# Optimization experiments

Hardware: AMD Instinct MI355X
Metric: run time of the kernel (lower is better)

Reference implementation:

```python
import jax, jax.numpy as jnp
import numpy as np


def setup_inputs() -> dict:
    key = jax.random.key(0)
    ks = jax.random.split(key, 8)
    B, C, H, W = 8, 256, 64, 64
    r = 32  # channels // reduction
    return {
        "x": jax.random.normal(ks[0], (B, C, H, W), dtype=jnp.float32),
        "wq": jax.random.normal(ks[1], (r, C), dtype=jnp.float32) * 0.02,
        "bq": jax.random.normal(ks[2], (r,), dtype=jnp.float32) * 0.02,
        "wk": jax.random.normal(ks[3], (r, C), dtype=jnp.float32) * 0.02,
        "bk": jax.random.normal(ks[4], (r,), dtype=jnp.float32) * 0.02,
        "wv": jax.random.normal(ks[5], (C, C), dtype=jnp.float32) * 0.02,
        "bv": jax.random.normal(ks[6], (C,), dtype=jnp.float32) * 0.02,
        "gamma": jax.random.normal(ks[7], (1,), dtype=jnp.float32),
    }


def reference(x, wq, bq, wk, bk, wv, bv, gamma):
    B, C, H, W = x.shape
    N = H * W
    r = wq.shape[0]
    scale = r ** (-0.5)
    xf = x.reshape(B, C, N)  # flatten spatial tokens
    # 1x1 convs == per-pixel linear projections
    q = jnp.einsum("rc,bcn->bnr", wq, xf) + bq  # (B, N, r)
    k = jnp.einsum("rc,bcn->brn", wk, xf) + bk[:, None]  # (B, r, N)
    v = jnp.einsum("dc,bcn->bdn", wv, xf) + bv[:, None]  # (B, C, N)
    attn = jax.nn.softmax(jnp.einsum("bnr,brm->bnm", q, k) * scale, axis=-1)  # (B, N, N)
    # out[b,c,n] = sum_m v[b,c,m] * attn[b,n,m]
    out = jnp.einsum("bdm,bnm->bdn", v, attn).reshape(B, C, H, W)
    return x + gamma[0] * out
```

## Files before the change

kernel.cpp:

```cpp
#include <hip/hip_runtime.h>
#include <hip/hip_bf16.h>


typedef float  f32x4   __attribute__((ext_vector_type(4)));
typedef short  short8  __attribute__((ext_vector_type(8)));
typedef unsigned short ushort4v __attribute__((ext_vector_type(4)));
typedef unsigned short ushort8v __attribute__((ext_vector_type(8)));

__device__ __forceinline__ unsigned short f2bf(float f) {
    __hip_bfloat16 h = __float2bfloat16(f);
    return __builtin_bit_cast(unsigned short, h);
}

__global__ __launch_bounds__(256) void wconv_kernel(
    const float* __restrict__ wq, const float* __restrict__ wk,
    const float* __restrict__ wv, unsigned short* __restrict__ Wall)
{
    int i4 = blockIdx.x * 256 + threadIdx.x;
    int e = i4 * 4;
    const float* src; int off;
    if (e < 8192)       { src = wq; off = e; }
    else if (e < 16384) { src = wk; off = e - 8192; }
    else                { src = wv; off = e - 16384; }
    f32x4 v = *(const f32x4*)(src + off);
    ushort4v u;
#pragma unroll
    for (int j = 0; j < 4; ++j) u[j] = f2bf(v[j]);
    *(ushort4v*)(Wall + e) = u;
}

__global__ __launch_bounds__(256) void xpose_kernel(
    const float* __restrict__ x, unsigned short* __restrict__ xT, int C, int N)
{
    const int t  = threadIdx.x;
    const int n  = blockIdx.x * 256 + t;
    const int c0 = blockIdx.y * 64;
    const int b  = blockIdx.z;
    const float* xb = x + ((size_t)b * C + c0) * N + n;

    unsigned short tmp[64];
#pragma unroll
    for (int i = 0; i < 64; ++i)
        tmp[i] = f2bf(xb[(size_t)i * N]);

    unsigned short* dst = xT + ((size_t)b * N + n) * 256 + c0;
#pragma unroll
    for (int i = 0; i < 8; ++i) {
        ushort8v u;
#pragma unroll
        for (int j = 0; j < 8; ++j) u[j] = tmp[i * 8 + j];
        *(ushort8v*)(dst + i * 8) = u;
    }
}

__global__ __launch_bounds__(256) void projmm_kernel(
    const unsigned short* __restrict__ xT,
    const unsigned short* __restrict__ Wall,
    const float* __restrict__ bq, const float* __restrict__ bk,
    const float* __restrict__ bv,
    unsigned short* __restrict__ qa,
    unsigned short* __restrict__ ka,
    unsigned char* __restrict__ vt8,
    int N, float scale)
{
    __shared__ __align__(16) unsigned short xs[64 * 136];
    __shared__ __align__(16) unsigned short ws[64 * 136];

    const int t  = threadIdx.x;
    const int l  = t & 63;
    const int w  = t >> 6;
    const int qi = l & 15;
    const int g  = l >> 4;
    const int n0 = blockIdx.x * 64;
    const int o0 = blockIdx.y * 64;
    const int b  = blockIdx.z;
    const int tile = n0 >> 6;
    const unsigned short* xTb = xT + (size_t)b * N * 256;

    const f32x4 zero4 = {0.f, 0.f, 0.f, 0.f};
    f32x4 acc[4];
#pragma unroll
    for (int nf = 0; nf < 4; ++nf) acc[nf] = zero4;

    for (int kp = 0; kp < 2; ++kp) {
        if (kp) __syncthreads();
        for (int it = w; it < 34; it += 4) {
            int isw = it >= 17;
            int it2 = isw ? it - 17 : it;
            unsigned short* lbase = (isw ? ws : xs) + it2 * 512;
            int ch  = it2 * 64 + l;
            int row = ch / 17;
            int c16 = ch - row * 17;
            int cc  = c16 > 15 ? 15 : c16;
            const unsigned short* src = isw
                ? (Wall + (size_t)(o0 + row) * 256 + kp * 128 + cc * 8)
                : (xTb + (size_t)(n0 + row) * 256 + kp * 128 + cc * 8);
            __builtin_amdgcn_global_load_lds(
                (const __attribute__((address_space(1))) unsigned int*)src,
                (__attribute__((address_space(3))) unsigned int*)lbase, 16, 0, 0);
        }
        __syncthreads();

#pragma unroll
        for (int ks = 0; ks < 4; ++ks) {
            short8 af;
            {
                const unsigned short* ap = ws + (w * 16 + qi) * 136 + ks * 32 + g * 4;
                ushort4v lo = *(const ushort4v*)ap;
                ushort4v hi = *(const ushort4v*)(ap + 16);
#pragma unroll
                for (int j = 0; j < 4; ++j) { af[j] = (short)lo[j]; af[4 + j] = (short)hi[j]; }
            }
#pragma unroll
            for (int nf = 0; nf < 4; ++nf) {
                short8 bf;
                const unsigned short* bp = xs + (nf * 16 + qi) * 136 + ks * 32 + g * 4;
                ushort4v lo = *(const ushort4v*)bp;
                ushort4v hi = *(const ushort4v*)(bp + 16);
#pragma unroll
                for (int j = 0; j < 4; ++j) { bf[j] = (short)lo[j]; bf[4 + j] = (short)hi[j]; }
                acc[nf] = __builtin_amdgcn_mfma_f32_16x16x32_bf16(af, bf, acc[nf], 0, 0, 0);
            }
        }
    }

    if (o0 == 0) {
        const float* bias = (w < 2) ? bq : bk;
        float sc = (w < 2) ? scale : 1.0f;
        unsigned short* dst = (w < 2) ? qa : ka;
#pragma unroll
        for (int nf = 0; nf < 4; ++nf) {
            ushort4v u;
#pragma unroll
            for (int j = 0; j < 4; ++j) {
                int r = (w & 1) * 16 + g * 4 + j;
                u[j] = f2bf((acc[nf][j] + bias[r]) * sc);
            }
            *(ushort4v*)(dst + ((((size_t)b * 64 + tile) * 4 + nf) * 64 + g * 16 + qi) * 8 + (w & 1) * 4) = u;
        }
    } else {
        unsigned char* vtb = vt8 + ((size_t)b * 64 + tile) * 16384;
#pragma unroll
        for (int nf = 0; nf < 4; ++nf) {
            int m = nf * 16 + qi;
            int G   = ((m & 32) ? 4 : 0) + ((m >> 2) & 3);
            int pos = ((m >> 4) & 1) * 4 + (m & 3);
#pragma unroll
            for (int j = 0; j < 4; ++j) {
                int c = o0 - 64 + w * 16 + g * 4 + j;
                int r = __builtin_amdgcn_cvt_pk_fp8_f32(acc[nf][j] + bv[c], 0.f, 0, false);
                vtb[(size_t)c * 64 + ((G ^ ((c >> 1) & 7)) << 3) + pos] = (unsigned char)(r & 0xFF);
            }
        }
    }
}

__global__ __launch_bounds__(512, 4) void attn_kernel(
    const float* __restrict__ x,
    const unsigned short* __restrict__ qa,
    const unsigned short* __restrict__ ka,
    const unsigned char* __restrict__ vt8,
    const float* __restrict__ gamma,
    float* __restrict__ out, int C, int N)
{
    __shared__ __align__(16) unsigned char vs[4][20480];

    const int t  = threadIdx.x;
    const int l  = t & 63;
    const int w  = t >> 6;
    const int qi = l & 15;
    const int g  = l >> 4;
    const int qg = w & 3;
    const int kh = w >> 2;
    const int tile_q = blockIdx.x;
    const int b  = blockIdx.y;

    const f32x4 zero4 = {0.f, 0.f, 0.f, 0.f};

    short8 qfrag = *(const short8*)(
        qa + ((((size_t)b * 64 + tile_q) * 4 + qg) * 64 + l) * 8);

    const unsigned char* kab_b = (const unsigned char*)(ka + ((size_t)b * 64) * 2048);
    const unsigned char* vtb   = vt8 + ((size_t)b * 64) * 16384;

    auto stage = [&](int buf, int tl) {
        const unsigned char* vsrc = vtb + (size_t)tl * 16384 + w * 2048 + l * 16;
        unsigned char* vdst = &vs[buf][w * 2048 + l * 16];
        __builtin_amdgcn_global_load_lds(
            (const __attribute__((address_space(1))) unsigned int*)vsrc,
            (__attribute__((address_space(3))) unsigned int*)vdst, 16, 0, 0);
        __builtin_amdgcn_global_load_lds(
            (const __attribute__((address_space(1))) unsigned int*)(vsrc + 1024),
            (__attribute__((address_space(3))) unsigned int*)(vdst + 1024), 16, 0, 0);
        const unsigned char* ksrc = kab_b + (size_t)tl * 4096 + w * 512 + l * 4;
        unsigned char* kdst = &vs[buf][16384 + w * 512 + l * 4];
        __builtin_amdgcn_global_load_lds(
            (const __attribute__((address_space(1))) unsigned int*)ksrc,
            (__attribute__((address_space(3))) unsigned int*)kdst, 4, 0, 0);
        __builtin_amdgcn_global_load_lds(
            (const __attribute__((address_space(1))) unsigned int*)(ksrc + 256),
            (__attribute__((address_space(3))) unsigned int*)(kdst + 256), 4, 0, 0);
    };

    f32x4 o_[16];
#pragma unroll
    for (int cf = 0; cf < 16; ++cf) o_[cf] = zero4;
    float lsum = 0.f;
    long acur = 0;

    auto packP = [&](const f32x4& s0, const f32x4& s1) -> long {
        float p[8];
#pragma unroll
        for (int j = 0; j < 4; ++j) { p[j] = __expf(s0[j]); p[4 + j] = __expf(s1[j]); }
#pragma unroll
        for (int j = 0; j < 8; ++j) lsum += p[j];
        int w0 = __builtin_amdgcn_cvt_pk_fp8_f32(p[0], p[1], 0, false);
        w0 = __builtin_amdgcn_cvt_pk_fp8_f32(p[2], p[3], w0, true);
        int w1 = __builtin_amdgcn_cvt_pk_fp8_f32(p[4], p[5], 0, false);
        w1 = __builtin_amdgcn_cvt_pk_fp8_f32(p[6], p[7], w1, true);
        return (long)(((unsigned long long)(unsigned int)w0) |
                      ((unsigned long long)(unsigned int)w1 << 32));
    };

    const int voff = (((kh << 2) | g) ^ ((qi >> 1) & 7)) << 3;
    auto pv = [&](int buf) {
        const unsigned char* vrow = &vs[buf][qi * 64 + voff];
#pragma unroll
        for (int cf = 0; cf < 16; ++cf) {
            long v8 = *(const long*)(vrow + cf * 1024);
            o_[cf] = __builtin_amdgcn_mfma_f32_16x16x32_fp8_fp8(acur, v8, o_[cf], 0, 0, 0);
        }
    };

    stage(0, 0);
    stage(1, 1);

    for (int tl = 0; tl < 64; ++tl) {
        asm volatile("s_waitcnt vmcnt(4)\n\ts_barrier" ::: "memory");
        __builtin_amdgcn_sched_barrier(0);

        if (tl < 62) stage((tl + 2) & 3, tl + 2);

        const unsigned char* kb2 = &vs[tl & 3][16384 + kh * 2048 + l * 16];
        short8 kf0 = *(const short8*)kb2;
        short8 kf1 = *(const short8*)(kb2 + 1024);
        f32x4 s0 = __builtin_amdgcn_mfma_f32_16x16x32_bf16(kf0, qfrag, zero4, 0, 0, 0);
        f32x4 s1 = __builtin_amdgcn_mfma_f32_16x16x32_bf16(kf1, qfrag, zero4, 0, 0, 0);

        if (tl) pv((tl - 1) & 3);

        acur = packP(s0, s1);
    }
    pv(3);

    float l_run = lsum;
    l_run += __shfl_xor(l_run, 16);
    l_run += __shfl_xor(l_run, 32);

    __syncthreads();
    float* cbuf = (float*)vs;
    float* lex  = cbuf + 8192;
    const int lx = l & 31;
    float* bp = cbuf + ((qg * 64) + l) * 32;
    if (kh == 1) {
        lex[qg * 64 + l] = l_run;
#pragma unroll
        for (int cf = 0; cf < 8; ++cf)
#pragma unroll
            for (int j = 0; j < 4; ++j) bp[(cf * 4 + j) ^ lx] = o_[cf][j];
    }
    __syncthreads();

    float cj[4];
    const float gm = gamma[0];
    const float* xb = x + (size_t)b * C * N;
    float* ob = out + (size_t)b * C * N;
    const int ncol = tile_q * 64 + qg * 16 + g * 4;

    if (kh == 0) {
        float lt = l_run + lex[qg * 64 + l];
        float c0 = gm / lt;
#pragma unroll
        for (int j = 0; j < 4; ++j) cj[j] = __shfl(c0, g * 4 + j);
#pragma unroll
        for (int cf = 0; cf < 8; ++cf) {
            int c = cf * 16 + qi;
            f32x4 xv = *(const f32x4*)(xb + (size_t)c * N + ncol);
            f32x4 ov;
#pragma unroll
            for (int j = 0; j < 4; ++j)
                ov[j] = xv[j] + (o_[cf][j] + bp[(cf * 4 + j) ^ lx]) * cj[j];
            *(f32x4*)(ob + (size_t)c * N + ncol) = ov;
        }
    }
    __syncthreads();

    if (kh == 1) {
#pragma unroll
        for (int cf = 0; cf < 8; ++cf)
#pragma unroll
            for (int j = 0; j < 4; ++j) bp[(cf * 4 + j) ^ lx] = o_[8 + cf][j];
    }
    __syncthreads();

    if (kh == 0) {
#pragma unroll
        for (int cf = 0; cf < 8; ++cf) {
            int c = (8 + cf) * 16 + qi;
            f32x4 xv = *(const f32x4*)(xb + (size_t)c * N + ncol);
            f32x4 ov;
#pragma unroll
            for (int j = 0; j < 4; ++j)
                ov[j] = xv[j] + (o_[8 + cf][j] + bp[(cf * 4 + j) ^ lx]) * cj[j];
            *(f32x4*)(ob + (size_t)c * N + ncol) = ov;
        }
    }
}

extern "C" void kernel_launch(void* const* d_in, const int* in_sizes, int n_in,
                              void* d_out, int out_size, void* d_ws, size_t ws_size,
                              hipStream_t stream) {
    const float* x     = (const float*)d_in[0];
    const float* wq    = (const float*)d_in[1];
    const float* bq    = (const float*)d_in[2];
    const float* wk    = (const float*)d_in[3];
    const float* bk    = (const float*)d_in[4];
    const float* wv    = (const float*)d_in[5];
    const float* bv    = (const float*)d_in[6];
    const float* gamma = (const float*)d_in[7];
    float* out = (float*)d_out;

    const int B = 8, C = 256, N = 4096;
    const float scale = 0.17677669529663687f;

    unsigned short* qa   = (unsigned short*)d_ws;
    unsigned short* ka   = qa + (size_t)B * 64 * 4 * 64 * 8;
    unsigned short* xT   = ka + (size_t)B * 64 * 4 * 64 * 8;
    unsigned short* Wall = xT + (size_t)B * N * 256;
    unsigned char*  vt8  = (unsigned char*)(Wall + 81920);

    wconv_kernel<<<80, 256, 0, stream>>>(wq, wk, wv, Wall);
    xpose_kernel<<<dim3(N / 256, C / 64, B), 256, 0, stream>>>(x, xT, C, N);
    projmm_kernel<<<dim3(N / 64, 5, B), 256, 0, stream>>>(
        xT, Wall, bq, bk, bv, qa, ka, vt8, N, scale);
    attn_kernel<<<dim3(N / 64, B), 512, 0, stream>>>(x, qa, ka, vt8, gamma, out, C, N);
}
```

Before: 109.7 us.

## Fuse x transpose/bf16 convert into projection kernel with double-buffered weights

Removes the separate transpose kernel and its bf16 xT intermediate buffer. The projection kernel now reads fp32 x directly, converts it to bf16 into a full-K shared tile, and loops over all five output blocks inside one workgroup. Weight tiles are double-buffered so the next slice loads while the current one is multiplied. The grid shrinks by 5x, which reduces parallelism, and the strided fp32 loads of x may coalesce less well.

```diff
diff --git a/kernel.cpp b/kernel.cpp
--- a/kernel.cpp
+++ b/kernel.cpp
@@ -29,32 +29,8 @@
     *(ushort4v*)(Wall + e) = u;
 }
 
-__global__ __launch_bounds__(256) void xpose_kernel(
-    const float* __restrict__ x, unsigned short* __restrict__ xT, int C, int N)
-{
-    const int t  = threadIdx.x;
-    const int n  = blockIdx.x * 256 + t;
-    const int c0 = blockIdx.y * 64;
-    const int b  = blockIdx.z;
-    const float* xb = x + ((size_t)b * C + c0) * N + n;
-
-    unsigned short tmp[64];
-#pragma unroll
-    for (int i = 0; i < 64; ++i)
-        tmp[i] = f2bf(xb[(size_t)i * N]);
-
-    unsigned short* dst = xT + ((size_t)b * N + n) * 256 + c0;
-#pragma unroll
-    for (int i = 0; i < 8; ++i) {
-        ushort8v u;
-#pragma unroll
-        for (int j = 0; j < 8; ++j) u[j] = tmp[i * 8 + j];
-        *(ushort8v*)(dst + i * 8) = u;
-    }
-}
-
 __global__ __launch_bounds__(256) void projmm_kernel(
-    const unsigned short* __restrict__ xT,
+    const float* __restrict__ x,
     const unsigned short* __restrict__ Wall,
     const float* __restrict__ bq, const float* __restrict__ bk,
     const float* __restrict__ bv,
@@ -63,8 +39,8 @@
     unsigned char* __restrict__ vt8,
     int N, float scale)
 {
-    __shared__ __align__(16) unsigned short xs[64 * 136];
-    __shared__ __align__(16) unsigned short ws[64 * 136];
+    __shared__ __align__(16) unsigned short xs[64 * 272];
+    __shared__ __align__(16) unsigned short ws2[2][64 * 136];
 
     const int t  = threadIdx.x;
     const int l  = t & 63;
@@ -72,40 +48,57 @@
     const int qi = l & 15;
     const int g  = l >> 4;
     const int n0 = blockIdx.x * 64;
-    const int o0 = blockIdx.y * 64;
-    const int b  = blockIdx.z;
+    const int b  = blockIdx.y;
     const int tile = n0 >> 6;
-    const unsigned short* xTb = xT + (size_t)b * N * 256;
-
-    const f32x4 zero4 = {0.f, 0.f, 0.f, 0.f};
-    f32x4 acc[4];
-#pragma unroll
-    for (int nf = 0; nf < 4; ++nf) acc[nf] = zero4;
-
-    for (int kp = 0; kp < 2; ++kp) {
-        if (kp) __syncthreads();
-        for (int it = w; it < 34; it += 4) {
-            int isw = it >= 17;
-            int it2 = isw ? it - 17 : it;
-            unsigned short* lbase = (isw ? ws : xs) + it2 * 512;
-            int ch  = it2 * 64 + l;
+
+    {
+        const float* xb = x + ((size_t)b * 256 + w * 64) * N + n0 + l;
+        unsigned short* dst = xs + l * 272 + w * 64;
+#pragma unroll
+        for (int i = 0; i < 8; ++i) {
+            ushort8v u;
+#pragma unroll
+            for (int j = 0; j < 8; ++j)
+                u[j] = f2bf(xb[(size_t)(i * 8 + j) * N]);
+            *(ushort8v*)(dst + i * 8) = u;
+        }
+    }
+
+    auto stageW = [&](int pb, int p) {
+        int ob = p >> 1, kp = p & 1;
+        for (int it = w; it < 17; it += 4) {
+            unsigned short* lbase = ws2[pb] + it * 512;
+            int ch  = it * 64 + l;
             int row = ch / 17;
             int c16 = ch - row * 17;
             int cc  = c16 > 15 ? 15 : c16;
-            const unsigned short* src = isw
-                ? (Wall + (size_t)(o0 + row) * 256 + kp * 128 + cc * 8)
-                : (xTb + (size_t)(n0 + row) * 256 + kp * 128 + cc * 8);
+            const unsigned short* src = Wall + (size_t)(ob * 64 + row) * 256 + kp * 128 + cc * 8;
             __builtin_amdgcn_global_load_lds(
                 (const __attribute__((address_space(1))) unsigned int*)src,
                 (__attribute__((address_space(3))) unsigned int*)lbase, 16, 0, 0);
         }
-        __syncthreads();
-
+    };
+
+    const f32x4 zero4 = {0.f, 0.f, 0.f, 0.f};
+    f32x4 acc[4];
+
+    stageW(0, 0);
+    __syncthreads();
+
+    for (int p = 0; p < 10; ++p) {
+        const int ob = p >> 1, kp = p & 1;
+        if (p < 9) stageW((p + 1) & 1, p + 1);
+        if (kp == 0) {
+#pragma unroll
+            for (int nf = 0; nf < 4; ++nf) acc[nf] = zero4;
+        }
+
+        const unsigned short* wsb = ws2[p & 1];
 #pragma unroll
         for (int ks = 0; ks < 4; ++ks) {
             short8 af;
             {
-                const unsigned short* ap = ws + (w * 16 + qi) * 136 + ks * 32 + g * 4;
+                const unsigned short* ap = wsb + (w * 16 + qi) * 136 + ks * 32 + g * 4;
                 ushort4v lo = *(const ushort4v*)ap;
                 ushort4v hi = *(const ushort4v*)(ap + 16);
 #pragma unroll
@@ -114,7 +107,7 @@
 #pragma unroll
             for (int nf = 0; nf < 4; ++nf) {
                 short8 bf;
-                const unsigned short* bp = xs + (nf * 16 + qi) * 136 + ks * 32 + g * 4;
+                const unsigned short* bp = xs + (nf * 16 + qi) * 272 + kp * 128 + ks * 32 + g * 4;
                 ushort4v lo = *(const ushort4v*)bp;
                 ushort4v hi = *(const ushort4v*)(bp + 16);
 #pragma unroll
@@ -122,36 +115,39 @@
                 acc[nf] = __builtin_amdgcn_mfma_f32_16x16x32_bf16(af, bf, acc[nf], 0, 0, 0);
             }
         }
-    }
-
-    if (o0 == 0) {
-        const float* bias = (w < 2) ? bq : bk;
-        float sc = (w < 2) ? scale : 1.0f;
-        unsigned short* dst = (w < 2) ? qa : ka;
-#pragma unroll
-        for (int nf = 0; nf < 4; ++nf) {
-            ushort4v u;
-#pragma unroll
-            for (int j = 0; j < 4; ++j) {
-                int r = (w & 1) * 16 + g * 4 + j;
-                u[j] = f2bf((acc[nf][j] + bias[r]) * sc);
+
+        if (kp == 1) {
+            if (ob == 0) {
+                const float* bias = (w < 2) ? bq : bk;
+                float sc = (w < 2) ? scale : 1.0f;
+                unsigned short* dst = (w < 2) ? qa : ka;
+#pragma unroll
+                for (int nf = 0; nf < 4; ++nf) {
+                    ushort4v u;
+#pragma unroll
+                    for (int j = 0; j < 4; ++j) {
+                        int r = (w & 1) * 16 + g * 4 + j;
+                        u[j] = f2bf((acc[nf][j] + bias[r]) * sc);
+                    }
+                    *(ushort4v*)(dst + ((((size_t)b * 64 + tile) * 4 + nf) * 64 + g * 16 + qi) * 8 + (w & 1) * 4) = u;
+                }
+            } else {
+                unsigned char* vtb = vt8 + ((size_t)b * 64 + tile) * 16384;
+#pragma unroll
+                for (int nf = 0; nf < 4; ++nf) {
+                    int m = nf * 16 + qi;
+                    int G   = ((m & 32) ? 4 : 0) + ((m >> 2) & 3);
+                    int pos = ((m >> 4) & 1) * 4 + (m & 3);
+#pragma unroll
+                    for (int j = 0; j < 4; ++j) {
+                        int c = (ob - 1) * 64 + w * 16 + g * 4 + j;
+                        int r = __builtin_amdgcn_cvt_pk_fp8_f32(acc[nf][j] + bv[c], 0.f, 0, false);
+                        vtb[(size_t)c * 64 + ((G ^ ((c >> 1) & 7)) << 3) + pos] = (unsigned char)(r & 0xFF);
+                    }
+                }
             }
-            *(ushort4v*)(dst + ((((size_t)b * 64 + tile) * 4 + nf) * 64 + g * 16 + qi) * 8 + (w & 1) * 4) = u;
-        }
-    } else {
-        unsigned char* vtb = vt8 + ((size_t)b * 64 + tile) * 16384;
-#pragma unroll
-        for (int nf = 0; nf < 4; ++nf) {
-            int m = nf * 16 + qi;
-            int G   = ((m & 32) ? 4 : 0) + ((m >> 2) & 3);
-            int pos = ((m >> 4) & 1) * 4 + (m & 3);
-#pragma unroll
-            for (int j = 0; j < 4; ++j) {
-                int c = o0 - 64 + w * 16 + g * 4 + j;
-                int r = __builtin_amdgcn_cvt_pk_fp8_f32(acc[nf][j] + bv[c], 0.f, 0, false);
-                vtb[(size_t)c * 64 + ((G ^ ((c >> 1) & 7)) << 3) + pos] = (unsigned char)(r & 0xFF);
-            }
-        }
+        }
+        __syncthreads();
     }
 }
 
@@ -335,13 +331,11 @@
 
     unsigned short* qa   = (unsigned short*)d_ws;
     unsigned short* ka   = qa + (size_t)B * 64 * 4 * 64 * 8;
-    unsigned short* xT   = ka + (size_t)B * 64 * 4 * 64 * 8;
-    unsigned short* Wall = xT + (size_t)B * N * 256;
+    unsigned short* Wall = ka + (size_t)B * 64 * 4 * 64 * 8;
     unsigned char*  vt8  = (unsigned char*)(Wall + 81920);
 
     wconv_kernel<<<80, 256, 0, stream>>>(wq, wk, wv, Wall);
-    xpose_kernel<<<dim3(N / 256, C / 64, B), 256, 0, stream>>>(x, xT, C, N);
-    projmm_kernel<<<dim3(N / 64, 5, B), 256, 0, stream>>>(
-        xT, Wall, bq, bk, bv, qa, ka, vt8, N, scale);
+    projmm_kernel<<<dim3(N / 64, B), 256, 0, stream>>>(
+        x, Wall, bq, bk, bv, qa, ka, vt8, N, scale);
     attn_kernel<<<dim3(N / 64, B), 512, 0, stream>>>(x, qa, ka, vt8, gamma, out, C, N);
 }
```

Result: no change. 111.1 us (+1.2%).
